# Kernel optimization log

Hardware: AMD Instinct MI355X
Metric: run time of the kernel (lower is better)

## Reference

```python
import jax, jax.numpy as jnp
import numpy as np

N = 131072   # nodes
C = 64       # in_channels
K = 32       # n_super_nodes
B = 16       # graphs in batch
EPS = 1e-9
TAU = 1.0


def setup_inputs() -> dict:
    key = jax.random.key(0)
    ks = jax.random.split(key, 8)
    x = jax.random.normal(ks[0], (N, C), dtype=jnp.float32)
    batch = jnp.sort(jax.random.randint(ks[1], (N,), 0, B)).astype(jnp.int32)
    pos = jax.random.normal(ks[2], (N, 2), dtype=jnp.float32)
    u = jax.random.uniform(ks[3], (N, K), dtype=jnp.float32)  # uniform noise for gumbel
    W1 = jax.random.normal(ks[4], (C, C), dtype=jnp.float32) / jnp.sqrt(C)
    b1 = jnp.zeros((C,), dtype=jnp.float32)
    W2 = jax.random.normal(ks[5], (C, K), dtype=jnp.float32) / jnp.sqrt(C)
    b2 = jnp.zeros((K,), dtype=jnp.float32)
    scaling = jnp.ones((1,), dtype=jnp.float32)
    active_mask = jnp.ones((K,), dtype=jnp.float32)
    return {"x": x, "batch": batch, "pos": pos, "u": u, "W1": W1, "b1": b1,
            "W2": W2, "b2": b2, "scaling": scaling, "active_mask": active_mask}


def reference(x, batch, pos, u, W1, b1, W2, b2, scaling, active_mask):
    # assignment MLP: Linear -> ReLU -> Linear, then learned scaling
    logits = (jax.nn.relu(x @ W1 + b1) @ W2 + b2) * scaling[0]  # [N, K]
    # eval-mode masking of inactive super-nodes
    logits = jnp.where(active_mask[None, :] == 0, -1e9, logits)
    # gumbel-softmax (soft, hard=False)
    g = -jnp.log(-jnp.log(u + EPS) + EPS)
    s = jax.nn.softmax((logits + g) / TAU, axis=-1)           # [N, K]

    avg_s = s.mean(axis=0)                                     # [K]
    entropy = -jnp.mean(jnp.sum(s * jnp.log(s + EPS), axis=1))
    diversity = jnp.sum(avg_s * jnp.log(avg_s + EPS))
    pruning = jnp.mean(jnp.abs(avg_s * (1.0 - active_mask)))
    sparsity = jnp.sum(active_mask) / K

    # global spatial variance of each super-node cluster
    s_sum = s.sum(axis=0, keepdims=True) + EPS                 # [1, K]
    s_norm = s / s_sum                                         # [N, K]
    mu_g = s_norm.T @ pos                                      # [K, 2]
    pos_sq = jnp.sum(pos ** 2, axis=1, keepdims=True)          # [N, 1]
    var = (s_norm.T @ pos_sq)[:, 0] - 2.0 * jnp.sum(mu_g * (s_norm.T @ pos), axis=1) \
          + jnp.sum(mu_g ** 2, axis=1)                         # [K]
    spatial = var.mean()

    # per-graph super-node centroids via scatter-sum over batch index
    sum_s_pos = jax.ops.segment_sum(pos[:, None, :] * s[:, :, None], batch,
                                    num_segments=B)            # [B, K, 2]
    sum_s = jax.ops.segment_sum(s, batch, num_segments=B)[..., None] + EPS  # [B, K, 1]
    mu = sum_s_pos / sum_s                                     # [B, K, 2]

    # pairwise separation (repulsion) among super-node centroids
    dist_sq = jnp.sum((mu[:, :, None, :] - mu[:, None, :, :]) ** 2, axis=-1)  # [B, K, K]
    eye = jnp.eye(K, dtype=mu.dtype)[None]
    separation = jnp.sum((1.0 / (dist_sq + 1.0)) * (1.0 - eye)) / (K * (K - 1) + EPS)

    # pooled features: outer product then scatter-sum  ->  [B, K, C]
    out = jax.ops.segment_sum(x[:, None, :] * s[:, :, None], batch, num_segments=B)

    return (out, s, entropy, diversity, spatial, pruning, sparsity, separation, mu)
```

## Files before the change

kernel.cpp:

```cpp
#include <hip/hip_runtime.h>

#define EPS 1e-9f
constexpr int NN = 131072;
constexpr int CD = 64;
constexpr int KK = 32;
constexpr int BB = 16;

constexpr int WS_ENT  = 0;
constexpr int WS_BACC = 16;
constexpr int FP      = 72;
constexpr int WS_BACC_SZ = BB * KK * FP;
constexpr int WS_W1T  = WS_BACC + WS_BACC_SZ;
constexpr int WS_TAG  = WS_W1T + 4096;
constexpr int WS_PART = WS_TAG + 1040;
constexpr int CELLS   = 68 * 32;

constexpr int OUT_OUT  = 0;
constexpr int OUT_S    = BB * KK * CD;
constexpr int OUT_SCAL = OUT_S + NN * KK;
constexpr int OUT_MU   = OUT_SCAL + 6;

__global__ void prep_k(const float* __restrict__ W1, float* __restrict__ ws) {
    int t = blockIdx.x * 256 + threadIdx.x;
    int c = t >> 6, j = t & 63;
    ws[WS_W1T + j * 64 + c] = W1[c * 64 + j];
}

__global__ __launch_bounds__(256, 2)
void node_k(const float* __restrict__ x,
            const float* __restrict__ u,
            const float* __restrict__ w1t,
            const float* __restrict__ b1,
            const float* __restrict__ W2,
            const float* __restrict__ b2,
            const float* __restrict__ scaling,
            const float* __restrict__ amask,
            float* __restrict__ s_out,
            float* __restrict__ ent_acc) {
    const int n = blockIdx.x * blockDim.x + threadIdx.x;
    const float* xr = x + n * 64;
    float xv[64];
#pragma unroll
    for (int c4 = 0; c4 < 16; c4++) {
        float4 v = *(const float4*)(xr + 4 * c4);
        xv[4 * c4 + 0] = v.x; xv[4 * c4 + 1] = v.y;
        xv[4 * c4 + 2] = v.z; xv[4 * c4 + 3] = v.w;
    }
    float logit[32];
#pragma unroll
    for (int k = 0; k < 32; k++) logit[k] = b2[k];
#pragma unroll 2
    for (int j = 0; j < 64; j++) {
        const float* w1r = w1t + j * 64;
        float p0 = b1[j], p1 = 0.f, p2 = 0.f, p3 = 0.f;
#pragma unroll
        for (int c = 0; c < 64; c += 4) {
            p0 = fmaf(xv[c + 0], w1r[c + 0], p0);
            p1 = fmaf(xv[c + 1], w1r[c + 1], p1);
            p2 = fmaf(xv[c + 2], w1r[c + 2], p2);
            p3 = fmaf(xv[c + 3], w1r[c + 3], p3);
        }
        float hj = fmaxf((p0 + p1) + (p2 + p3), 0.f);
        const float* w2r = W2 + j * 32;
#pragma unroll
        for (int k = 0; k < 32; k++) logit[k] = fmaf(hj, w2r[k], logit[k]);
    }
    const float sc = scaling[0];
    const float* ur = u + n * 32;
    float m = -3.0e38f;
#pragma unroll
    for (int k4 = 0; k4 < 8; k4++) {
        float4 uv = *(const float4*)(ur + 4 * k4);
        float us[4] = {uv.x, uv.y, uv.z, uv.w};
#pragma unroll
        for (int q = 0; q < 4; q++) {
            const int k = 4 * k4 + q;
            float l = logit[k] * sc;
            l = (amask[k] == 0.f) ? -1e9f : l;
            float g = -__logf(-__logf(us[q] + EPS) + EPS);
            float z = l + g;
            logit[k] = z;
            m = fmaxf(m, z);
        }
    }
    float e0 = 0.f, e1 = 0.f, e2 = 0.f, e3 = 0.f;
#pragma unroll
    for (int k = 0; k < 32; k += 4) {
        float a = __expf(logit[k] - m);     logit[k] = a;     e0 += a;
        float b = __expf(logit[k + 1] - m); logit[k + 1] = b; e1 += b;
        float c = __expf(logit[k + 2] - m); logit[k + 2] = c; e2 += c;
        float d = __expf(logit[k + 3] - m); logit[k + 3] = d; e3 += d;
    }
    const float inv = 1.f / ((e0 + e1) + (e2 + e3));
    float ent = 0.f;
#pragma unroll
    for (int k = 0; k < 32; k++) {
        float sv = logit[k] * inv;
        logit[k] = sv;
        ent += sv * __logf(sv + EPS);
    }
    float* so = s_out + n * 32;
#pragma unroll
    for (int k4 = 0; k4 < 8; k4++)
        *(float4*)(so + 4 * k4) = make_float4(logit[4 * k4], logit[4 * k4 + 1],
                                              logit[4 * k4 + 2], logit[4 * k4 + 3]);
#pragma unroll
    for (int off = 32; off > 0; off >>= 1) ent += __shfl_down(ent, off, 64);
    if ((threadIdx.x & 63) == 0) atomicAdd(ent_acc, ent);
}

__global__ void pool_k(const float* __restrict__ s,
                       const float* __restrict__ x,
                       const float* __restrict__ pos,
                       const int* __restrict__ batch,
                       float* __restrict__ bacc,
                       float* __restrict__ part,
                       int* __restrict__ tags,
                       int npb) {
    const int t = threadIdx.x;
    const int k = t & 31;
    const int fg = t >> 5;
    const int base = blockIdx.x * npb;
    float acc[8];
    float accx = 0.f;
#pragma unroll
    for (int f = 0; f < 8; f++) acc[f] = 0.f;
    int cur_b = batch[base];
#pragma unroll 2
    for (int n = base; n < base + npb; n++) {
        const int b = batch[n];
        if (b != cur_b) {
            float* dst = bacc + (cur_b * 32 + k) * FP;
#pragma unroll
            for (int f = 0; f < 8; f++) { atomicAdd(dst + fg * 8 + f, acc[f]); acc[f] = 0.f; }
            if (fg < 4) { atomicAdd(dst + 64 + fg, accx); accx = 0.f; }
            cur_b = b;
        }
        const float sv = s[n * 32 + k];
        const float4 v0 = *(const float4*)(x + n * 64 + fg * 8);
        const float4 v1 = *(const float4*)(x + n * 64 + fg * 8 + 4);
        acc[0] = fmaf(sv, v0.x, acc[0]);
        acc[1] = fmaf(sv, v0.y, acc[1]);
        acc[2] = fmaf(sv, v0.z, acc[2]);
        acc[3] = fmaf(sv, v0.w, acc[3]);
        acc[4] = fmaf(sv, v1.x, acc[4]);
        acc[5] = fmaf(sv, v1.y, acc[5]);
        acc[6] = fmaf(sv, v1.z, acc[6]);
        acc[7] = fmaf(sv, v1.w, acc[7]);
        if (fg < 4) {
            float2 p = *(const float2*)(pos + n * 2);
            float e = (fg == 0) ? p.x : (fg == 1) ? p.y
                    : (fg == 2) ? (p.x * p.x + p.y * p.y) : 1.f;
            accx = fmaf(sv, e, accx);
        }
    }
    float* pp = part + (size_t)blockIdx.x * CELLS;
#pragma unroll
    for (int f = 0; f < 8; f++) pp[(fg * 8 + f) * 32 + k] = acc[f];
    if (fg < 4) pp[(64 + fg) * 32 + k] = accx;
    if (t == 0) tags[blockIdx.x] = cur_b;
}

__global__ void reduce_k(const float* __restrict__ part,
                         const int* __restrict__ tags,
                         float* __restrict__ bacc,
                         float* __restrict__ outp,
                         int nblk) {
    const int b = blockIdx.x;
    const int cell = blockIdx.y * 256 + threadIdx.x;
    if (cell >= CELLS) return;
    const int k = cell & 31, f = cell >> 5;
    int lo = 0, hi = nblk;
    while (lo < hi) { int mid = (lo + hi) >> 1; if (tags[mid] < b) lo = mid + 1; else hi = mid; }
    int lo2 = lo, hi2 = nblk;
    while (lo2 < hi2) { int mid = (lo2 + hi2) >> 1; if (tags[mid] < b + 1) lo2 = mid + 1; else hi2 = mid; }
    float v = 0.f;
    for (int blk = lo; blk < lo2; blk++)
        v += part[(size_t)blk * CELLS + cell];
    const int idx = (b * 32 + k) * FP + f;
    const float tot = bacc[idx] + v;
    bacc[idx] = tot;
    if (f < 64) outp[OUT_OUT + ((b * 32 + k) << 6) + f] = tot;
}

__global__ void fin_k(const float* __restrict__ ws,
                      const float* __restrict__ amask,
                      float* __restrict__ outp) {
    const int t = threadIdx.x;
    const float* bacc = ws + WS_BACC;
    __shared__ float mu_s[BB * KK * 2];
    for (int idx = t; idx < BB * KK * 2; idx += 256) {
        int bk = idx >> 1, d = idx & 1;
        float v = bacc[bk * FP + 64 + d] / (bacc[bk * FP + 67] + EPS);
        mu_s[idx] = v;
        outp[OUT_MU + idx] = v;
    }
    __shared__ float kred[32][4];
    if (t < 32) {
        float S = 0, px = 0, py = 0, sq = 0;
        for (int b = 0; b < 16; b++) {
            const float* pp = bacc + (b * 32 + t) * FP;
            S += pp[67]; px += pp[64]; py += pp[65]; sq += pp[66];
        }
        float avg = S / (float)NN;
        float am = amask[t];
        float ssum = S + EPS;
        float mx = px / ssum, my = py / ssum;
        kred[t][0] = avg * __logf(avg + EPS);
        kred[t][1] = fabsf(avg * (1.f - am));
        kred[t][2] = sq / ssum - mx * mx - my * my;
        kred[t][3] = am;
    }
    __syncthreads();
    float sep = 0.f;
    for (int idx = t; idx < BB * KK * KK; idx += 256) {
        int b = idx >> 10, i = (idx >> 5) & 31, j = idx & 31;
        if (i != j) {
            float dx = mu_s[(b * 32 + i) * 2 + 0] - mu_s[(b * 32 + j) * 2 + 0];
            float dy = mu_s[(b * 32 + i) * 2 + 1] - mu_s[(b * 32 + j) * 2 + 1];
            sep += 1.f / (dx * dx + dy * dy + 1.f);
        }
    }
    __shared__ float red[256];
    red[t] = sep;
    __syncthreads();
    for (int s2 = 128; s2 > 0; s2 >>= 1) {
        if (t < s2) red[t] += red[t + s2];
        __syncthreads();
    }
    if (t == 0) {
        float div = 0, pru = 0, spa = 0, spar = 0;
        for (int kq = 0; kq < 32; kq++) {
            div += kred[kq][0]; pru += kred[kq][1];
            spa += kred[kq][2]; spar += kred[kq][3];
        }
        outp[OUT_SCAL + 0] = -ws[WS_ENT] / (float)NN;
        outp[OUT_SCAL + 1] = div;
        outp[OUT_SCAL + 2] = spa / 32.f;
        outp[OUT_SCAL + 3] = pru / 32.f;
        outp[OUT_SCAL + 4] = spar / 32.f;
        outp[OUT_SCAL + 5] = red[0] / (32.f * 31.f + EPS);
    }
}

extern "C" void kernel_launch(void* const* d_in, const int* in_sizes, int n_in,
                              void* d_out, int out_size, void* d_ws, size_t ws_size,
                              hipStream_t stream) {
    const float* x       = (const float*)d_in[0];
    const int*   batch   = (const int*)d_in[1];
    const float* pos     = (const float*)d_in[2];
    const float* u       = (const float*)d_in[3];
    const float* W1      = (const float*)d_in[4];
    const float* b1      = (const float*)d_in[5];
    const float* W2      = (const float*)d_in[6];
    const float* b2      = (const float*)d_in[7];
    const float* scaling = (const float*)d_in[8];
    const float* amask   = (const float*)d_in[9];
    float* outp = (float*)d_out;
    float* ws   = (float*)d_ws;

    int npb = 128;
    while (npb < NN &&
           ws_size < ((size_t)WS_PART + (size_t)(NN / npb) * CELLS) * sizeof(float))
        npb <<= 1;
    const int nblk = NN / npb;

    hipMemsetAsync(ws, 0, (size_t)(WS_BACC + WS_BACC_SZ) * sizeof(float), stream);
    prep_k<<<16, 256, 0, stream>>>(W1, ws);
    node_k<<<NN / 256, 256, 0, stream>>>(x, u, ws + WS_W1T, b1, W2, b2, scaling, amask,
                                         outp + OUT_S, ws + WS_ENT);
    pool_k<<<nblk, 256, 0, stream>>>(outp + OUT_S, x, pos, batch,
                                     ws + WS_BACC, ws + WS_PART, (int*)(ws + WS_TAG), npb);
    reduce_k<<<dim3(BB, (CELLS + 255) / 256), 256, 0, stream>>>(
        ws + WS_PART, (const int*)(ws + WS_TAG), ws + WS_BACC, outp, nblk);
    fin_k<<<1, 256, 0, stream>>>(ws, amask, outp);
}
```

Baseline: 264.9 us.

## Stage x tile in padded LDS with coalesced loads, shrink node_k blocks to 128

node_k now loads each block's 128x64 slice of x into shared memory using coalesced float4 loads, with rows padded to a stride of 68. In the first-layer dot product each thread reads its row from LDS instead of holding 64 x values in registers. The old per-thread row loads were strided and uncoalesced, and the 64-float register array limited occupancy. In exchange the kernel adds about 34KB of LDS per block, which caps blocks per CU, plus a barrier, and it reloads x from LDS once per hidden unit j.

```diff
diff --git a/kernel.cpp b/kernel.cpp
--- a/kernel.cpp
+++ b/kernel.cpp
@@ -26,7 +26,8 @@
     ws[WS_W1T + j * 64 + c] = W1[c * 64 + j];
 }
 
-__global__ __launch_bounds__(256, 2)
+constexpr int XS_STRIDE = 68;
+__global__ __launch_bounds__(128)
 void node_k(const float* __restrict__ x,
             const float* __restrict__ u,
             const float* __restrict__ w1t,
@@ -37,15 +38,19 @@
             const float* __restrict__ amask,
             float* __restrict__ s_out,
             float* __restrict__ ent_acc) {
-    const int n = blockIdx.x * blockDim.x + threadIdx.x;
-    const float* xr = x + n * 64;
-    float xv[64];
-#pragma unroll
-    for (int c4 = 0; c4 < 16; c4++) {
-        float4 v = *(const float4*)(xr + 4 * c4);
-        xv[4 * c4 + 0] = v.x; xv[4 * c4 + 1] = v.y;
-        xv[4 * c4 + 2] = v.z; xv[4 * c4 + 3] = v.w;
-    }
+    __shared__ float xs[128 * XS_STRIDE];
+    const int t = threadIdx.x;
+    const float4* gx = (const float4*)(x + (size_t)blockIdx.x * 128 * 64);
+#pragma unroll
+    for (int i = 0; i < 16; i++) {
+        const int f = i * 128 + t;
+        const int row = f >> 4, c4 = f & 15;
+        *(float4*)(xs + row * XS_STRIDE + c4 * 4) = gx[f];
+    }
+    __syncthreads();
+
+    const int n = blockIdx.x * 128 + t;
+    const float* xr = xs + t * XS_STRIDE;
     float logit[32];
 #pragma unroll
     for (int k = 0; k < 32; k++) logit[k] = b2[k];
@@ -54,11 +59,12 @@
         const float* w1r = w1t + j * 64;
         float p0 = b1[j], p1 = 0.f, p2 = 0.f, p3 = 0.f;
 #pragma unroll
-        for (int c = 0; c < 64; c += 4) {
-            p0 = fmaf(xv[c + 0], w1r[c + 0], p0);
-            p1 = fmaf(xv[c + 1], w1r[c + 1], p1);
-            p2 = fmaf(xv[c + 2], w1r[c + 2], p2);
-            p3 = fmaf(xv[c + 3], w1r[c + 3], p3);
+        for (int c4 = 0; c4 < 16; c4++) {
+            float4 xq = *(const float4*)(xr + c4 * 4);
+            p0 = fmaf(xq.x, w1r[c4 * 4 + 0], p0);
+            p1 = fmaf(xq.y, w1r[c4 * 4 + 1], p1);
+            p2 = fmaf(xq.z, w1r[c4 * 4 + 2], p2);
+            p3 = fmaf(xq.w, w1r[c4 * 4 + 3], p3);
         }
         float hj = fmaxf((p0 + p1) + (p2 + p3), 0.f);
         const float* w2r = W2 + j * 32;
@@ -106,7 +112,7 @@
                                               logit[4 * k4 + 2], logit[4 * k4 + 3]);
 #pragma unroll
     for (int off = 32; off > 0; off >>= 1) ent += __shfl_down(ent, off, 64);
-    if ((threadIdx.x & 63) == 0) atomicAdd(ent_acc, ent);
+    if ((t & 63) == 0) atomicAdd(ent_acc, ent);
 }
 
 __global__ void pool_k(const float* __restrict__ s,
@@ -267,7 +273,7 @@
 
     hipMemsetAsync(ws, 0, (size_t)(WS_BACC + WS_BACC_SZ) * sizeof(float), stream);
     prep_k<<<16, 256, 0, stream>>>(W1, ws);
-    node_k<<<NN / 256, 256, 0, stream>>>(x, u, ws + WS_W1T, b1, W2, b2, scaling, amask,
+    node_k<<<NN / 128, 128, 0, stream>>>(x, u, ws + WS_W1T, b1, W2, b2, scaling, amask,
                                          outp + OUT_S, ws + WS_ENT);
     pool_k<<<nblk, 256, 0, stream>>>(outp + OUT_S, x, pos, batch,
                                      ws + WS_BACC, ws + WS_PART, (int*)(ws + WS_TAG), npb);
```

New measurement: 269.6 us. Within noise of the previous version (+1.8%).

## Restructure node MLP into hidden-unit blocks to cut registers and drop W1 transpose

Applied to the files above, without the earlier changes.

The first MLP layer now processes hidden units in blocks of 16. It re-reads x from memory for each block instead of holding all 64 input values in registers, and reads W1 directly in its original layout, so the separate transpose kernel and its workspace are removed. Launch bounds are raised to request 4 blocks per SM, aiming for higher occupancy to hide memory and uniform-load latency. In exchange, x is read four times per node (likely served from cache), and the compiler may spill registers under the tighter bound.

```diff
diff --git a/kernel.cpp b/kernel.cpp
--- a/kernel.cpp
+++ b/kernel.cpp
@@ -10,8 +10,7 @@
 constexpr int WS_BACC = 16;
 constexpr int FP      = 72;
 constexpr int WS_BACC_SZ = BB * KK * FP;
-constexpr int WS_W1T  = WS_BACC + WS_BACC_SZ;
-constexpr int WS_TAG  = WS_W1T + 4096;
+constexpr int WS_TAG  = WS_BACC + WS_BACC_SZ;
 constexpr int WS_PART = WS_TAG + 1040;
 constexpr int CELLS   = 68 * 32;
 
@@ -20,16 +19,10 @@
 constexpr int OUT_SCAL = OUT_S + NN * KK;
 constexpr int OUT_MU   = OUT_SCAL + 6;
 
-__global__ void prep_k(const float* __restrict__ W1, float* __restrict__ ws) {
-    int t = blockIdx.x * 256 + threadIdx.x;
-    int c = t >> 6, j = t & 63;
-    ws[WS_W1T + j * 64 + c] = W1[c * 64 + j];
-}
-
-__global__ __launch_bounds__(256, 2)
+__global__ __launch_bounds__(256, 4)
 void node_k(const float* __restrict__ x,
             const float* __restrict__ u,
-            const float* __restrict__ w1t,
+            const float* __restrict__ W1,
             const float* __restrict__ b1,
             const float* __restrict__ W2,
             const float* __restrict__ b2,
@@ -37,36 +30,41 @@
             const float* __restrict__ amask,
             float* __restrict__ s_out,
             float* __restrict__ ent_acc) {
-    const int n = blockIdx.x * blockDim.x + threadIdx.x;
-    const float* xr = x + n * 64;
-    float xv[64];
-#pragma unroll
-    for (int c4 = 0; c4 < 16; c4++) {
-        float4 v = *(const float4*)(xr + 4 * c4);
-        xv[4 * c4 + 0] = v.x; xv[4 * c4 + 1] = v.y;
-        xv[4 * c4 + 2] = v.z; xv[4 * c4 + 3] = v.w;
-    }
+    const int n = blockIdx.x * 256 + threadIdx.x;
+    const float* xr = x + (size_t)n * 64;
     float logit[32];
 #pragma unroll
     for (int k = 0; k < 32; k++) logit[k] = b2[k];
-#pragma unroll 2
-    for (int j = 0; j < 64; j++) {
-        const float* w1r = w1t + j * 64;
-        float p0 = b1[j], p1 = 0.f, p2 = 0.f, p3 = 0.f;
-#pragma unroll
-        for (int c = 0; c < 64; c += 4) {
-            p0 = fmaf(xv[c + 0], w1r[c + 0], p0);
-            p1 = fmaf(xv[c + 1], w1r[c + 1], p1);
-            p2 = fmaf(xv[c + 2], w1r[c + 2], p2);
-            p3 = fmaf(xv[c + 3], w1r[c + 3], p3);
-        }
-        float hj = fmaxf((p0 + p1) + (p2 + p3), 0.f);
-        const float* w2r = W2 + j * 32;
-#pragma unroll
-        for (int k = 0; k < 32; k++) logit[k] = fmaf(hj, w2r[k], logit[k]);
-    }
+
+    for (int jb = 0; jb < 4; jb++) {
+        float h[16];
+#pragma unroll
+        for (int jj = 0; jj < 16; jj++) h[jj] = b1[jb * 16 + jj];
+#pragma unroll
+        for (int c4 = 0; c4 < 16; c4++) {
+            const float4 xq = *(const float4*)(xr + c4 * 4);
+            const float xs4[4] = {xq.x, xq.y, xq.z, xq.w};
+#pragma unroll
+            for (int q = 0; q < 4; q++) {
+                const float xc = xs4[q];
+                const float* w1r = W1 + (c4 * 4 + q) * 64 + jb * 16;
+#pragma unroll
+                for (int jj = 0; jj < 16; jj++)
+                    h[jj] = fmaf(xc, w1r[jj], h[jj]);
+            }
+        }
+#pragma unroll
+        for (int jj = 0; jj < 16; jj++) {
+            const float hj = fmaxf(h[jj], 0.f);
+            const float* w2r = W2 + (jb * 16 + jj) * 32;
+#pragma unroll
+            for (int k = 0; k < 32; k++)
+                logit[k] = fmaf(hj, w2r[k], logit[k]);
+        }
+    }
+
     const float sc = scaling[0];
-    const float* ur = u + n * 32;
+    const float* ur = u + (size_t)n * 32;
     float m = -3.0e38f;
 #pragma unroll
     for (int k4 = 0; k4 < 8; k4++) {
@@ -99,7 +97,7 @@
         logit[k] = sv;
         ent += sv * __logf(sv + EPS);
     }
-    float* so = s_out + n * 32;
+    float* so = s_out + (size_t)n * 32;
 #pragma unroll
     for (int k4 = 0; k4 < 8; k4++)
         *(float4*)(so + 4 * k4) = make_float4(logit[4 * k4], logit[4 * k4 + 1],
@@ -266,8 +264,7 @@
     const int nblk = NN / npb;
 
     hipMemsetAsync(ws, 0, (size_t)(WS_BACC + WS_BACC_SZ) * sizeof(float), stream);
-    prep_k<<<16, 256, 0, stream>>>(W1, ws);
-    node_k<<<NN / 256, 256, 0, stream>>>(x, u, ws + WS_W1T, b1, W2, b2, scaling, amask,
+    node_k<<<NN / 256, 256, 0, stream>>>(x, u, W1, b1, W2, b2, scaling, amask,
                                          outp + OUT_S, ws + WS_ENT);
     pool_k<<<nblk, 256, 0, stream>>>(outp + OUT_S, x, pos, batch,
                                      ws + WS_BACC, ws + WS_PART, (int*)(ws + WS_TAG), npb);
```

Result: faster. 246.0 us (-7.1%).
